# Kernel optimization log

Hardware: AMD Instinct MI355X
Metric: run time of the kernel (lower is better)

Reference implementation:

```python
import jax, jax.numpy as jnp
import numpy as np

TAU = 0.01

def setup_inputs() -> dict:
    key = jax.random.key(0)
    k1, k2, k3 = jax.random.split(key, 3)
    HW, C, H, W = 9216, 256, 96, 96
    x_feature = jax.random.normal(k1, (HW, C), dtype=jnp.float32)
    y_feature = jax.random.normal(k2, (HW, C), dtype=jnp.float32)
    ref = jax.random.uniform(k3, (1, 3, H, W), dtype=jnp.float32)
    return {"x_feature": x_feature, "y_feature": y_feature, "ref": ref}

def _normalize(f):
    # per-channel: subtract mean over pixels, divide by L2 norm over pixels
    # (both computed on the ORIGINAL f, matching the torch single-expression semantics)
    return (f - f.mean(axis=0)) / jnp.linalg.norm(f, axis=0)

def reference(x_feature, y_feature, ref):
    h, w = ref.shape[2], ref.shape[3]
    xn = _normalize(x_feature)          # [HW, C]
    yn = _normalize(y_feature)          # [HW, C]
    corr = jnp.einsum('qc,kc->qk', xn, yn)          # [HW, HW] correlation
    ref_ab = ref[0, 1:].reshape(2, -1).T            # [HW, 2] ab colors
    attn = jax.nn.softmax(corr / TAU, axis=1)
    warped_color = attn @ ref_ab                    # [HW, 2]
    confidence = corr.max(axis=1)                   # [HW]
    W_out = warped_color.T.reshape(1, 2, h, w)
    S_out = confidence.reshape(1, 1, h, w)
    return (W_out, S_out)
```

## Files before the change

### kernel.cpp

```cpp
#include <hip/hip_runtime.h>
#include <hip/hip_bf16.h>

#define HW_N 9216
#define CH 256
#define KBLK 32
#define SCALE2 144.269504089f
#define INV_SCALE2 6.93147180559945e-3f

typedef __attribute__((ext_vector_type(8))) short bf16x8;
typedef __attribute__((ext_vector_type(4))) float f32x4;

__device__ inline unsigned short f2b(float f) {
    unsigned u = __builtin_bit_cast(unsigned, f);
    u += 0x7FFF + ((u >> 16) & 1);
    return (unsigned short)(u >> 16);
}

__global__ void stats_partial(const float* __restrict__ x,
                              const float* __restrict__ y,
                              float* __restrict__ part) {
    int c = threadIdx.x;
    int r0 = blockIdx.x * 128;
    float xs = 0.f, xq = 0.f, ys = 0.f, yq = 0.f;
    for (int r = r0; r < r0 + 128; ++r) {
        float xv = x[(size_t)r * CH + c]; xs += xv; xq += xv * xv;
        float yv = y[(size_t)r * CH + c]; ys += yv; yq += yv * yv;
    }
    float* p = part + (size_t)blockIdx.x * 1024;
    p[c] = xs; p[256 + c] = xq; p[512 + c] = ys; p[768 + c] = yq;
}

__global__ void stats_final(const float* __restrict__ part, float* __restrict__ stats) {
    int c = threadIdx.x;
    float xs = 0.f, xq = 0.f, ys = 0.f, yq = 0.f;
    for (int b = 0; b < 72; ++b) {
        const float* p = part + (size_t)b * 1024;
        xs += p[c]; xq += p[256 + c]; ys += p[512 + c]; yq += p[768 + c];
    }
    stats[c]       = xs / (float)HW_N;
    stats[256 + c] = SCALE2 / sqrtf(xq);
    stats[512 + c] = ys / (float)HW_N;
    stats[768 + c] = 1.0f / sqrtf(yq);
}

__global__ void normalize_k(const float* __restrict__ x,
                            const float* __restrict__ y,
                            const float* __restrict__ stats,
                            unsigned short* __restrict__ xn,
                            unsigned short* __restrict__ ynP) {
    int idx = (blockIdx.x * 256 + threadIdx.x) * 8;
    int c = idx & (CH - 1);
    const float* src = blockIdx.y ? y : x;
    const float* st = stats + blockIdx.y * 512;
    float4 v0 = *(const float4*)(src + idx);
    float4 v1 = *(const float4*)(src + idx + 4);
    float f[8] = {v0.x, v0.y, v0.z, v0.w, v1.x, v1.y, v1.z, v1.w};
    bf16x8 o;
#pragma unroll
    for (int j = 0; j < 8; ++j)
        o[j] = (short)f2b((f[j] - st[c + j]) * st[256 + c + j]);
    if (blockIdx.y == 0) {
        *(bf16x8*)(xn + idx) = o;
    } else {
        int key = idx >> 8;
        int dst = (key >> 4) * 4096 + (c >> 5) * 512 + ((c & 31) >> 3) * 128 + (key & 15) * 8;
        *(bf16x8*)(ynP + dst) = o;
    }
}

__launch_bounds__(256, 2)
__global__ void attn_k(const unsigned short* __restrict__ xn,
                       const unsigned short* __restrict__ ynP,
                       const float* __restrict__ refimg,
                       float* __restrict__ part, int nsplit) {
    int tid = threadIdx.x;
    int lane = tid & 63, wave = tid >> 6;
    int l15 = lane & 15, l16 = lane >> 4;

    int chunk = gridDim.x >> 3;
    int wg = (blockIdx.x & 7) * chunk + (blockIdx.x >> 3);
    int bx = wg % 72, by = wg / 72;
    int qb = bx * 128 + wave * 32;
    int keys_per_split = HW_N / nsplit;
    int key0 = by * keys_per_split;
    int ntile = keys_per_split / KBLK;

    bf16x8 a[2][8];
#pragma unroll
    for (int qs = 0; qs < 2; ++qs) {
        const unsigned short* xrow = xn + (size_t)(qb + qs * 16 + l15) * CH + l16 * 8;
#pragma unroll
        for (int kk = 0; kk < 8; ++kk) a[qs][kk] = *(const bf16x8*)(xrow + kk * 32);
    }

    float M[2][4], den[2][4], nA[2][4], nB[2][4];
#pragma unroll
    for (int qs = 0; qs < 2; ++qs)
#pragma unroll
        for (int i = 0; i < 4; ++i) {
            M[qs][i] = -1e30f; den[qs][i] = 0.f; nA[qs][i] = 0.f; nB[qs][i] = 0.f;
        }

    const float* refA = refimg + HW_N;
    const float* refB = refimg + 2 * HW_N;
    const char* ypb = (const char*)ynP + ((size_t)(key0 >> 4) << 13) + lane * 16;

    for (int t = 0; t < ntile; ++t) {
        int kb = key0 + t * KBLK;
        const char* seg = ypb + ((size_t)t << 14);

        bf16x8 b0[8], b1[8];
#pragma unroll
        for (int kk = 0; kk < 8; ++kk) {
            b0[kk] = *(const bf16x8*)(seg + kk * 1024);
            b1[kk] = *(const bf16x8*)(seg + 8192 + kk * 1024);
        }
        float va0 = refA[kb + l15],      vb0 = refB[kb + l15];
        float va1 = refA[kb + 16 + l15], vb1 = refB[kb + 16 + l15];

        f32x4 acc0[2], acc1[2];
#pragma unroll
        for (int ct = 0; ct < 2; ++ct) {
            acc0[ct] = (f32x4){0.f, 0.f, 0.f, 0.f};
            acc1[ct] = (f32x4){0.f, 0.f, 0.f, 0.f};
        }
        __builtin_amdgcn_s_setprio(1);
#pragma unroll
        for (int kk = 0; kk < 8; ++kk) {
            acc0[0] = __builtin_amdgcn_mfma_f32_16x16x32_bf16(a[0][kk], b0[kk], acc0[0], 0, 0, 0);
            acc1[0] = __builtin_amdgcn_mfma_f32_16x16x32_bf16(a[1][kk], b0[kk], acc1[0], 0, 0, 0);
            acc0[1] = __builtin_amdgcn_mfma_f32_16x16x32_bf16(a[0][kk], b1[kk], acc0[1], 0, 0, 0);
            acc1[1] = __builtin_amdgcn_mfma_f32_16x16x32_bf16(a[1][kk], b1[kk], acc1[1], 0, 0, 0);
        }
        __builtin_amdgcn_s_setprio(0);

#pragma unroll
        for (int qs = 0; qs < 2; ++qs)
#pragma unroll
            for (int i = 0; i < 4; ++i) {
                float c0 = qs ? acc1[0][i] : acc0[0][i];
                float c1 = qs ? acc1[1][i] : acc0[1][i];
                M[qs][i] = fmaxf(M[qs][i], fmaxf(c0, c1));
                float p0 = exp2f(c0);
                float p1 = exp2f(c1);
                den[qs][i] += p0 + p1;
                nA[qs][i] += p0 * va0 + p1 * va1;
                nB[qs][i] += p0 * vb0 + p1 * vb1;
            }
    }

#pragma unroll
    for (int qs = 0; qs < 2; ++qs)
#pragma unroll
        for (int i = 0; i < 4; ++i) {
#pragma unroll
            for (int off = 1; off < 16; off <<= 1) {
                M[qs][i]   = fmaxf(M[qs][i], __shfl_xor(M[qs][i], off, 64));
                den[qs][i] += __shfl_xor(den[qs][i], off, 64);
                nA[qs][i]  += __shfl_xor(nA[qs][i], off, 64);
                nB[qs][i]  += __shfl_xor(nB[qs][i], off, 64);
            }
        }
    if (l15 == 0) {
#pragma unroll
        for (int qs = 0; qs < 2; ++qs)
#pragma unroll
            for (int i = 0; i < 4; ++i) {
                int q = qb + qs * 16 + l16 * 4 + i;
                float* p = part + ((size_t)by * HW_N + q) * 4;
                p[0] = M[qs][i]; p[1] = den[qs][i]; p[2] = nA[qs][i]; p[3] = nB[qs][i];
            }
    }
}

__global__ void combine_k(const float* __restrict__ part, float* __restrict__ out,
                          int nsplit) {
    int q = blockIdx.x * 256 + threadIdx.x;
    float M = -1e30f, den = 0.f, nA = 0.f, nB = 0.f;
    for (int s = 0; s < nsplit; ++s) {
        const float* p = part + ((size_t)s * HW_N + q) * 4;
        M = fmaxf(M, p[0]); den += p[1]; nA += p[2]; nB += p[3];
    }
    out[q]            = nA / den;
    out[HW_N + q]     = nB / den;
    out[2 * HW_N + q] = M * INV_SCALE2;
}

extern "C" void kernel_launch(void* const* d_in, const int* in_sizes, int n_in,
                              void* d_out, int out_size, void* d_ws, size_t ws_size,
                              hipStream_t stream) {
    (void)in_sizes; (void)n_in; (void)out_size;
    const float* x   = (const float*)d_in[0];
    const float* y   = (const float*)d_in[1];
    const float* ref = (const float*)d_in[2];
    float* out = (float*)d_out;

    char* ws = (char*)d_ws;
    unsigned short* xn  = (unsigned short*)ws;
    unsigned short* ynP = (unsigned short*)(ws + 4718592);
    float* partA = (float*)ws;
    float* stats = (float*)(ws + 2 * 4718592);
    float* partS = (float*)(ws + 2 * 4718592 + 4096);

    size_t base = 2 * 4718592 + 4096;
    int nsplit = (ws_size >= base + (size_t)12 * HW_N * 16) ? 12 : 6;

    hipLaunchKernelGGL(stats_partial, dim3(72), dim3(256), 0, stream, x, y, partA);
    hipLaunchKernelGGL(stats_final, dim3(1), dim3(256), 0, stream, partA, stats);
    hipLaunchKernelGGL(normalize_k, dim3(1152, 2), dim3(256), 0, stream, x, y, stats, xn, ynP);
    hipLaunchKernelGGL(attn_k, dim3(72 * nsplit), dim3(256), 0, stream, xn, ynP, ref, partS, nsplit);
    hipLaunchKernelGGL(combine_k, dim3(36), dim3(256), 0, stream, partS, out, nsplit);
}
```

Before: 99.71 us.

## Software-pipeline attention loop: prefetch next key tile, overlap softmax with MFMA

Restructures the attention main loop into a two-stage, double-buffered pipeline. While the MFMAs for the current 32-key tile run, the next tile's y-feature fragments and reference colours are loaded, and the online softmax of the previous tile's scores is interleaved with them. The loop is unrolled by two with even/odd register buffers, plus a prologue and epilogue. It also replaces exp2f with a raw v_exp_f32 and drops the s_setprio hints. The aim is to hide global-load latency and the exp/FMA work behind matrix instructions, at the cost of roughly doubling B-fragment and accumulator register use.

```diff
diff --git a/kernel.cpp b/kernel.cpp
--- a/kernel.cpp
+++ b/kernel.cpp
@@ -14,6 +14,10 @@
     unsigned u = __builtin_bit_cast(unsigned, f);
     u += 0x7FFF + ((u >> 16) & 1);
     return (unsigned short)(u >> 16);
+}
+
+__device__ inline float fexp2(float x) {
+    float r; asm("v_exp_f32 %0, %1" : "=v"(r) : "v"(x)); return r;
 }
 
 __global__ void stats_partial(const float* __restrict__ x,
@@ -68,6 +72,61 @@
     }
 }
 
+template<bool HAVE_NEXT, bool HAVE_PREV>
+__device__ __forceinline__ void tile_step(
+    const bf16x8 (&a)[2][8],
+    const bf16x8 (&bC0)[8], const bf16x8 (&bC1)[8],
+    f32x4 (&accC0)[2], f32x4 (&accC1)[2],
+    const f32x4 (&accP0)[2], const f32x4 (&accP1)[2],
+    float pva0, float pva1, float pvb0, float pvb1,
+    bf16x8 (&bN0)[8], bf16x8 (&bN1)[8], const char* segN,
+    float (&M)[2][4], float (&den)[2][4], float (&nA)[2][4], float (&nB)[2][4])
+{
+    accC0[0] = (f32x4){0.f,0.f,0.f,0.f}; accC0[1] = (f32x4){0.f,0.f,0.f,0.f};
+    accC1[0] = (f32x4){0.f,0.f,0.f,0.f}; accC1[1] = (f32x4){0.f,0.f,0.f,0.f};
+#pragma unroll
+    for (int kk = 0; kk < 8; ++kk) {
+        accC0[0] = __builtin_amdgcn_mfma_f32_16x16x32_bf16(a[0][kk], bC0[kk], accC0[0], 0, 0, 0);
+        accC1[0] = __builtin_amdgcn_mfma_f32_16x16x32_bf16(a[1][kk], bC0[kk], accC1[0], 0, 0, 0);
+        accC0[1] = __builtin_amdgcn_mfma_f32_16x16x32_bf16(a[0][kk], bC1[kk], accC0[1], 0, 0, 0);
+        accC1[1] = __builtin_amdgcn_mfma_f32_16x16x32_bf16(a[1][kk], bC1[kk], accC1[1], 0, 0, 0);
+        if constexpr (HAVE_NEXT) {
+            bN0[kk] = *(const bf16x8*)(segN + kk * 1024);
+            bN1[kk] = *(const bf16x8*)(segN + 8192 + kk * 1024);
+        }
+        if constexpr (HAVE_PREV) {
+            constexpr int qs_[8] = {0,0,0,0,1,1,1,1};
+            const int qs = qs_[kk], i = kk & 3;
+            float c0 = qs ? accP1[0][i] : accP0[0][i];
+            float c1 = qs ? accP1[1][i] : accP0[1][i];
+            M[qs][i] = fmaxf(fmaxf(M[qs][i], c0), c1);
+            float p0 = fexp2(c0), p1 = fexp2(c1);
+            den[qs][i] += p0 + p1;
+            nA[qs][i] += p0 * pva0 + p1 * pva1;
+            nB[qs][i] += p0 * pvb0 + p1 * pvb1;
+        }
+    }
+}
+
+__device__ __forceinline__ void softmax_tile(
+    const f32x4 (&P0)[2], const f32x4 (&P1)[2],
+    float va0, float va1, float vb0, float vb1,
+    float (&M)[2][4], float (&den)[2][4], float (&nA)[2][4], float (&nB)[2][4])
+{
+#pragma unroll
+    for (int qs = 0; qs < 2; ++qs)
+#pragma unroll
+        for (int i = 0; i < 4; ++i) {
+            float c0 = qs ? P1[0][i] : P0[0][i];
+            float c1 = qs ? P1[1][i] : P0[1][i];
+            M[qs][i] = fmaxf(fmaxf(M[qs][i], c0), c1);
+            float p0 = fexp2(c0), p1 = fexp2(c1);
+            den[qs][i] += p0 + p1;
+            nA[qs][i] += p0 * va0 + p1 * va1;
+            nB[qs][i] += p0 * vb0 + p1 * vb1;
+        }
+}
+
 __launch_bounds__(256, 2)
 __global__ void attn_k(const unsigned short* __restrict__ xn,
                        const unsigned short* __restrict__ ynP,
@@ -103,51 +162,44 @@
 
     const float* refA = refimg + HW_N;
     const float* refB = refimg + 2 * HW_N;
-    const char* ypb = (const char*)ynP + ((size_t)(key0 >> 4) << 13) + lane * 16;
-
-    for (int t = 0; t < ntile; ++t) {
-        int kb = key0 + t * KBLK;
-        const char* seg = ypb + ((size_t)t << 14);
-
-        bf16x8 b0[8], b1[8];
-#pragma unroll
-        for (int kk = 0; kk < 8; ++kk) {
-            b0[kk] = *(const bf16x8*)(seg + kk * 1024);
-            b1[kk] = *(const bf16x8*)(seg + 8192 + kk * 1024);
-        }
-        float va0 = refA[kb + l15],      vb0 = refB[kb + l15];
-        float va1 = refA[kb + 16 + l15], vb1 = refB[kb + 16 + l15];
-
-        f32x4 acc0[2], acc1[2];
-#pragma unroll
-        for (int ct = 0; ct < 2; ++ct) {
-            acc0[ct] = (f32x4){0.f, 0.f, 0.f, 0.f};
-            acc1[ct] = (f32x4){0.f, 0.f, 0.f, 0.f};
-        }
-        __builtin_amdgcn_s_setprio(1);
-#pragma unroll
-        for (int kk = 0; kk < 8; ++kk) {
-            acc0[0] = __builtin_amdgcn_mfma_f32_16x16x32_bf16(a[0][kk], b0[kk], acc0[0], 0, 0, 0);
-            acc1[0] = __builtin_amdgcn_mfma_f32_16x16x32_bf16(a[1][kk], b0[kk], acc1[0], 0, 0, 0);
-            acc0[1] = __builtin_amdgcn_mfma_f32_16x16x32_bf16(a[0][kk], b1[kk], acc0[1], 0, 0, 0);
-            acc1[1] = __builtin_amdgcn_mfma_f32_16x16x32_bf16(a[1][kk], b1[kk], acc1[1], 0, 0, 0);
-        }
-        __builtin_amdgcn_s_setprio(0);
-
-#pragma unroll
-        for (int qs = 0; qs < 2; ++qs)
-#pragma unroll
-            for (int i = 0; i < 4; ++i) {
-                float c0 = qs ? acc1[0][i] : acc0[0][i];
-                float c1 = qs ? acc1[1][i] : acc0[1][i];
-                M[qs][i] = fmaxf(M[qs][i], fmaxf(c0, c1));
-                float p0 = exp2f(c0);
-                float p1 = exp2f(c1);
-                den[qs][i] += p0 + p1;
-                nA[qs][i] += p0 * va0 + p1 * va1;
-                nB[qs][i] += p0 * vb0 + p1 * vb1;
-            }
-    }
+    const char* seg = (const char*)ynP + ((size_t)(key0 >> 4) << 13) + lane * 16;
+
+    bf16x8 bE0[8], bE1[8], bO0[8], bO1[8];
+    f32x4 aE0[2], aE1[2], aO0[2], aO1[2];
+    float eva0, eva1, evb0, evb1, ova0, ova1, ovb0, ovb1;
+
+#pragma unroll
+    for (int kk = 0; kk < 8; ++kk) {
+        bE0[kk] = *(const bf16x8*)(seg + kk * 1024);
+        bE1[kk] = *(const bf16x8*)(seg + 8192 + kk * 1024);
+    }
+    eva0 = refA[key0 + l15];      evb0 = refB[key0 + l15];
+    eva1 = refA[key0 + 16 + l15]; evb1 = refB[key0 + 16 + l15];
+
+    tile_step<true, false>(a, bE0, bE1, aE0, aE1, aO0, aO1, 0, 0, 0, 0,
+                           bO0, bO1, seg + 16384, M, den, nA, nB);
+    ova0 = refA[key0 + KBLK + l15];      ovb0 = refB[key0 + KBLK + l15];
+    ova1 = refA[key0 + KBLK + 16 + l15]; ovb1 = refB[key0 + KBLK + 16 + l15];
+
+    for (int t = 1; t + 1 < ntile; t += 2) {
+        tile_step<true, true>(a, bO0, bO1, aO0, aO1, aE0, aE1,
+                              eva0, eva1, evb0, evb1,
+                              bE0, bE1, seg + (size_t)(t + 1) * 16384, M, den, nA, nB);
+        { int kb = key0 + (t + 1) * KBLK;
+          eva0 = refA[kb + l15];      evb0 = refB[kb + l15];
+          eva1 = refA[kb + 16 + l15]; evb1 = refB[kb + 16 + l15]; }
+        tile_step<true, true>(a, bE0, bE1, aE0, aE1, aO0, aO1,
+                              ova0, ova1, ovb0, ovb1,
+                              bO0, bO1, seg + (size_t)(t + 2) * 16384, M, den, nA, nB);
+        { int kb = key0 + (t + 2) * KBLK;
+          ova0 = refA[kb + l15];      ovb0 = refB[kb + l15];
+          ova1 = refA[kb + 16 + l15]; ovb1 = refB[kb + 16 + l15]; }
+    }
+
+    tile_step<false, true>(a, bO0, bO1, aO0, aO1, aE0, aE1,
+                           eva0, eva1, evb0, evb1,
+                           bE0, bE1, nullptr, M, den, nA, nB);
+    softmax_tile(aO0, aO1, ova0, ova1, ovb0, ovb1, M, den, nA, nB);
 
 #pragma unroll
     for (int qs = 0; qs < 2; ++qs)
```

After: 127.3 us. +27.6%, slower.
